# Kernel tuning notes

Hardware: AMD Instinct MI355X
Metric: run time of the kernel (lower is better)

Reference implementation:

```python
import jax, jax.numpy as jnp
import numpy as np

B, S, C, H, W = 4, 32, 128, 16, 32
HID = 128
DEPTH = 2


def conv2d_same(x, w, b):
    # x: [B,Cin,H,W], w: [Cout,Cin,3,3] -> [B,Cout,H,W]
    y = jax.lax.conv_general_dilated(x, w, window_strides=(1, 1), padding='SAME',
                                     dimension_numbers=('NCHW', 'OIHW', 'NCHW'))
    return y + b[None, :, None, None]


def setup_inputs() -> dict:
    key = jax.random.key(0)
    ks = jax.random.split(key, 12)
    sc = 0.02
    x = jax.random.normal(ks[0], (B, S, C, H, W), dtype=jnp.float32)
    # stacked ConvLSTM cell params; input to each cell is C==HID channels
    conv_w = sc * jax.random.normal(ks[1], (DEPTH, 4 * HID, C + HID, 3, 3), dtype=jnp.float32)
    conv_b = jnp.zeros((DEPTH, 4 * HID), dtype=jnp.float32)
    init_h = 0.01 * jax.random.normal(ks[2], (DEPTH, HID), dtype=jnp.float32)
    init_c = 0.01 * jax.random.normal(ks[3], (DEPTH, HID), dtype=jnp.float32)
    fc_w = sc * jax.random.normal(ks[4], (C, HID), dtype=jnp.float32)
    fc_b = jnp.zeros((C,), dtype=jnp.float32)
    fco_w = sc * jax.random.normal(ks[5], (1, C), dtype=jnp.float32)
    fco_b = jnp.zeros((1,), dtype=jnp.float32)
    fca_w = sc * jax.random.normal(ks[6], (1, C), dtype=jnp.float32)
    fca_b = jnp.zeros((1,), dtype=jnp.float32)
    return dict(x=x, conv_w=conv_w, conv_b=conv_b, init_h=init_h, init_c=init_c,
                fc_w=fc_w, fc_b=fc_b, fco_w=fco_w, fco_b=fco_b, fca_w=fca_w, fca_b=fca_b)


def _forward(x, conv_w, conv_b, init_h, init_c, fc_w, fc_b, fco_w, fco_b, fca_w, fca_b):
    b, s, c, h, w = x.shape
    hid = init_h.shape[1]
    xs = jnp.moveaxis(x, 1, 0)  # [S,B,C,H,W] time-major for scan
    for d in range(conv_w.shape[0]):  # fixed small depth loop
        wd, bd = conv_w[d], conv_b[d]
        h0 = jnp.broadcast_to(init_h[d][None, :, None, None], (b, hid, h, w))
        c0 = jnp.broadcast_to(init_c[d][None, :, None, None], (b, hid, h, w))

        def step(carry, x_t):
            hs, cs = carry
            z = conv2d_same(jnp.concatenate([x_t, hs], axis=1), wd, bd)
            zi, zf, zg, zo = jnp.split(z, 4, axis=1)  # gate order i,f,g,o
            cs = jax.nn.sigmoid(zf) * cs + jax.nn.sigmoid(zi) * jnp.tanh(zg)
            hs = jax.nn.sigmoid(zo) * jnp.tanh(cs)
            return (hs, cs), hs

        _, xs = jax.lax.scan(step, (h0, c0), xs)
    # global average pool over H,W then heads
    feat = jnp.moveaxis(xs.mean(axis=(3, 4)), 0, 1)  # [B,S,HID]
    feat = jax.nn.relu(feat @ fc_w.T + fc_b)
    offset = feat @ fco_w.T + fco_b  # [B,S,1]
    angle = feat @ fca_w.T + fca_b   # [B,S,1]
    return offset, angle


def reference(x, conv_w, conv_b, init_h, init_c, fc_w, fc_b, fco_w, fco_b, fca_w, fca_b):
    return _forward(x, conv_w, conv_b, init_h, init_c, fc_w, fc_b, fco_w, fco_b, fca_w, fca_b)
```

## Files before the change

kernel.cpp:

```cpp
#include <hip/hip_runtime.h>

#define BB 4
#define SS 32
#define CC 128
#define HH 16
#define WW 32
#define HID 128
#define DEPTH 2
#define CIN 256
#define COUT 512
#define K9 (CIN * 9)
#define KH 1152
#define KFULL (2 * KH)
#define HW (HH * WW)
#define MM (BB * HW)
#define ACT (BB * HW * 128)

typedef __attribute__((ext_vector_type(4))) float f32x4;
typedef __attribute__((ext_vector_type(8))) short bf16x8;

static __device__ __forceinline__ unsigned short f2bf(float f) {
    union { float f; unsigned u; } v; v.f = f;
    unsigned r = v.u + 0x7FFF + ((v.u >> 16) & 1);
    return (unsigned short)(r >> 16);
}
static __device__ __forceinline__ float bf2f(unsigned short h) {
    union { float f; unsigned u; } v; v.u = ((unsigned)h) << 16; return v.f;
}

__global__ void transpose_w_kernel(const float* __restrict__ w,
                                   unsigned short* __restrict__ wh) {
    int idx = blockIdx.x * 256 + threadIdx.x;
    if (idx >= DEPTH * K9 * COUT) return;
    int n = idx % COUT;
    int k = (idx / COUT) % K9;
    int d = idx / (COUT * K9);
    int cin = k / 9, tap = k % 9;
    float v = w[(((long)(d * COUT + n) * CIN + cin) * 9) + tap];
    int row = (cin < CC) ? (tap * CC + cin) : (KH + tap * HID + (cin - CC));
    int g = n >> 7, r = n & 127;
    int ng = (r >> 4) * 64 + g * 16 + (r & 15);
    wh[((long)d * COUT + ng) * KFULL + row] = f2bf(v);
}

__global__ void pack_x_kernel(const float* __restrict__ x,
                              unsigned* __restrict__ xh32) {
    __shared__ unsigned lh[128 * 33];
    const int tid = threadIdx.x;
    const int sb  = blockIdx.x;
    const int s   = sb >> 2;
    const int b   = sb & 3;
    const int hw0 = blockIdx.y * 64;
    const float* src = x + ((long)(b * SS + s) * CC) * HW;

    #pragma unroll
    for (int it = 0; it < 16; ++it) {
        int cc = it * 8 + (tid >> 5);
        int hw = (tid & 31) * 2;
        float2 v = *(const float2*)&src[cc * HW + hw0 + hw];
        unsigned short h0 = f2bf(v.x), h1 = f2bf(v.y);
        lh[cc * 33 + (hw >> 1)] = (unsigned)h0 | ((unsigned)h1 << 16);
    }
    __syncthreads();
    const unsigned short* lhs = (const unsigned short*)lh;
    #pragma unroll
    for (int it = 0; it < 16; ++it) {
        int hw = it * 4 + (tid >> 6);
        int c2 = tid & 63;
        unsigned short a0 = lhs[(2 * c2) * 66 + hw];
        unsigned short a1 = lhs[(2 * c2 + 1) * 66 + hw];
        long o = ((long)sb * HW + hw0 + hw) * 64 + c2;
        xh32[o] = (unsigned)a0 | ((unsigned)a1 << 16);
    }
}

__global__ void init_state_kernel(const float* __restrict__ ih, const float* __restrict__ ic,
                                  unsigned short* __restrict__ hh,
                                  float* __restrict__ c, int d) {
    int idx = blockIdx.x * 256 + threadIdx.x;
    int hid = idx & 127;
    hh[idx] = f2bf(ih[d * HID + hid]);
    c[idx] = ic[d * HID + hid];
}

__global__ void zero_kernel(unsigned* __restrict__ zp) { zp[threadIdx.x] = 0u; }

__launch_bounds__(256)
__global__ void step_dual(
    const unsigned short* __restrict__ x1h, const unsigned short* __restrict__ h1h,
    float* __restrict__ c1, unsigned short* __restrict__ o1h,
    const unsigned short* __restrict__ x2h, const unsigned short* __restrict__ h2h,
    float* __restrict__ c2, unsigned short* __restrict__ o2h,
    const unsigned short* __restrict__ wh,
    const float* __restrict__ bias, const unsigned short* __restrict__ zp,
    int do1, int do2)
{
    __shared__ __align__(16) unsigned short lds[2][16384];

    const int bid  = blockIdx.x;
    const int xcd  = bid & 7;
    const int q    = bid >> 3;
    const int mblk = q & 31;
    const int pp   = xcd + ((q >> 5) << 3);
    const int nblk = pp & 7;
    const int z    = pp >> 3;
    if (z == 0) { if (!do1) return; } else { if (!do2) return; }

    const unsigned short* axh = z ? x2h : x1h;
    const unsigned short* ahh = z ? h2h : h1h;
    const unsigned short* wph = wh + (long)z * COUT * KFULL;
    const float* bsel  = bias + z * COUT;
    float* csel        = z ? c2 : c1;
    unsigned short* ohh = z ? o2h : o1h;

    const int m0   = mblk * 64;
    const int n0g  = nblk * 64;
    const int hid0 = nblk * 16;
    const int tid  = threadIdx.x;
    const int lane = tid & 63;
    const int wv   = tid >> 6;
    const int wm   = (wv >> 1) * 32;
    const int wn   = (wv & 1) * 32;
    const int b    = m0 >> 9;
    const int hwl  = m0 & 511;
    const int y0   = hwl >> 5;
    const long bhw = (long)b * HW;

    int sy_[4], sx_[4], ax_[4];
    long bro_[4];
    #pragma unroll
    for (int s = 0; s < 4; ++s) {
        int row = wv * 16 + s * 4 + (lane >> 4);
        int jx  = (lane & 15) ^ (row & 7);
        sx_[s] = row & 31;
        sy_[s] = y0 + (row >> 5);
        ax_[s] = jx * 8;
        bro_[s] = (long)(n0g + row) * KFULL + jx * 8;
    }

#define ISSUE(tt, pb) do {                                                        \
        const int _tt = (tt);                                                     \
        const int _tap = (_tt < 9) ? _tt : _tt - 9;                               \
        const unsigned short* _sh = (_tt < 9) ? axh : ahh;                        \
        const int _ky = _tap / 3 - 1;                                             \
        const int _kx = _tap - (_tap / 3) * 3 - 1;                                \
        const long _bk = (long)_tt * 128;                                         \
        _Pragma("unroll")                                                         \
        for (int _s = 0; _s < 4; ++_s) {                                          \
            int _yy = sy_[_s] + _ky, _xq = sx_[_s] + _kx;                         \
            bool _ok = (unsigned)_yy < (unsigned)HH && (unsigned)_xq < (unsigned)WW;\
            long _a = ((bhw + _yy * WW + _xq) << 7) + ax_[_s];                    \
            __builtin_amdgcn_global_load_lds(                                     \
                (const unsigned int*)(_ok ? _sh + _a : zp),                       \
                (unsigned int*)&lds[pb][wv * 2048 + _s * 512], 16, 0, 0);         \
            __builtin_amdgcn_global_load_lds(                                     \
                (const unsigned int*)(wph + bro_[_s] + _bk),                      \
                (unsigned int*)&lds[pb][8192 + wv * 2048 + _s * 512], 16, 0, 0);  \
        }                                                                         \
    } while (0)

    f32x4 acc00 = (f32x4){0.f,0.f,0.f,0.f};
    f32x4 acc01 = (f32x4){0.f,0.f,0.f,0.f};
    f32x4 acc10 = (f32x4){0.f,0.f,0.f,0.f};
    f32x4 acc11 = (f32x4){0.f,0.f,0.f,0.f};

    const int fr  = lane & 15;
    const int kqi = lane >> 4;
    const int am0 = wm + fr;
    const int am1 = wm + 16 + fr;
    const int bn0 = wn + fr;
    const int bn1 = wn + 16 + fr;

#define COMPUTE(P) do {                                                                   \
        const unsigned short* L = &lds[P][0];                                             \
        __builtin_amdgcn_s_setprio(1);                                                    \
        _Pragma("unroll")                                                                 \
        for (int s2 = 0; s2 < 4; ++s2) {                                                  \
            const int ca = s2 * 4 + kqi;                                 \
            bf16x8 fa0 = *(const bf16x8*)&L[am0 * 128 + ((ca ^ (am0 & 7)) << 3)];         \
            bf16x8 fa1 = *(const bf16x8*)&L[am1 * 128 + ((ca ^ (am1 & 7)) << 3)];         \
            bf16x8 fb0 = *(const bf16x8*)&L[8192 + bn0 * 128 + ((ca ^ (bn0 & 7)) << 3)];  \
            bf16x8 fb1 = *(const bf16x8*)&L[8192 + bn1 * 128 + ((ca ^ (bn1 & 7)) << 3)];  \
            acc00 = __builtin_amdgcn_mfma_f32_16x16x32_bf16(fa0, fb0, acc00, 0, 0, 0);    \
            acc01 = __builtin_amdgcn_mfma_f32_16x16x32_bf16(fa0, fb1, acc01, 0, 0, 0);    \
            acc10 = __builtin_amdgcn_mfma_f32_16x16x32_bf16(fa1, fb0, acc10, 0, 0, 0);    \
            acc11 = __builtin_amdgcn_mfma_f32_16x16x32_bf16(fa1, fb1, acc11, 0, 0, 0);    \
        }                                                                                 \
        __builtin_amdgcn_s_setprio(0);                                                    \
    } while (0)

    ISSUE(0, 0);
    __syncthreads();

    int p = 0;
    for (int tt = 0; tt < 18; ++tt) {
        if (tt + 1 < 18) ISSUE(tt + 1, 1 - p);
        COMPUTE(p);
        __syncthreads();
        p ^= 1;
    }

#undef ISSUE
#undef COMPUTE

    float* zt = (float*)&lds[0][0];
    {
        const int rm = (lane >> 4) * 4;
        const int cn = lane & 15;
        *(float4*)&zt[(wn + cn) * 68 + wm + rm]           = *(float4*)&acc00;
        *(float4*)&zt[(wn + 16 + cn) * 68 + wm + rm]      = *(float4*)&acc01;
        *(float4*)&zt[(wn + cn) * 68 + wm + 16 + rm]      = *(float4*)&acc10;
        *(float4*)&zt[(wn + 16 + cn) * 68 + wm + 16 + rm] = *(float4*)&acc11;
    }
    __syncthreads();

    {
        const int m    = tid & 63;
        const int jset = tid >> 6;
        float g[4][4];
        #pragma unroll
        for (int ji = 0; ji < 4; ++ji) {
            int jh = jset * 4 + ji;
            #pragma unroll
            for (int gi = 0; gi < 4; ++gi)
                g[ji][gi] = zt[(gi * 16 + jh) * 68 + m] + bsel[gi * 128 + hid0 + jh];
        }
        long base = ((long)b * HW + hwl + m) * 128 + hid0 + jset * 4;
        f32x4 cv = *(const f32x4*)&csel[base];
        float hv[4];
        #pragma unroll
        for (int ji = 0; ji < 4; ++ji) {
            float si = 1.f / (1.f + expf(-g[ji][0]));
            float sf = 1.f / (1.f + expf(-g[ji][1]));
            float so = 1.f / (1.f + expf(-g[ji][3]));
            float cs = sf * cv[ji] + si * tanhf(g[ji][2]);
            cv[ji] = cs;
            hv[ji] = so * tanhf(cs);
        }
        *(f32x4*)&csel[base] = cv;
        uint2 hp;
        hp.x = (unsigned)f2bf(hv[0]) | ((unsigned)f2bf(hv[1]) << 16);
        hp.y = (unsigned)f2bf(hv[2]) | ((unsigned)f2bf(hv[3]) << 16);
        *(uint2*)&ohh[base] = hp;
    }
}

__global__ void pool_kernel(const unsigned short* __restrict__ s2h,
                            float* __restrict__ pooled) {
    int bs = blockIdx.x;
    int j  = threadIdx.x;
    const unsigned short* ph = s2h + (long)bs * HW * 128 + j;
    float sum = 0.f;
    #pragma unroll 8
    for (int hw = 0; hw < HW; ++hw)
        sum += bf2f(ph[hw * 128]);
    pooled[bs * HID + j] = sum * (1.f / HW);
}

__global__ void head_kernel(const float* __restrict__ pooled,
                            const float* __restrict__ fc_w, const float* __restrict__ fc_b,
                            const float* __restrict__ fco_w, const float* __restrict__ fco_b,
                            const float* __restrict__ fca_w, const float* __restrict__ fca_b,
                            float* __restrict__ out) {
    int bs = blockIdx.x;
    int b  = bs / SS;
    int s  = bs % SS;
    int j  = threadIdx.x;
    const float* prow = pooled + (long)(s * BB + b) * HID;
    float acc = fc_b[j];
    #pragma unroll 4
    for (int k = 0; k < HID; ++k) acc += fc_w[j * HID + k] * prow[k];
    float f = fmaxf(acc, 0.f);
    __shared__ float ro[128], ra[128];
    ro[j] = f * fco_w[j];
    ra[j] = f * fca_w[j];
    __syncthreads();
    for (int off = 64; off; off >>= 1) {
        if (j < off) { ro[j] += ro[j + off]; ra[j] += ra[j + off]; }
        __syncthreads();
    }
    if (j == 0) {
        out[bs]           = ro[0] + fco_b[0];
        out[BB * SS + bs] = ra[0] + fca_b[0];
    }
}

extern "C" void kernel_launch(void* const* d_in, const int* in_sizes, int n_in,
                              void* d_out, int out_size, void* d_ws, size_t ws_size,
                              hipStream_t stream) {
    const float* x      = (const float*)d_in[0];
    const float* conv_w = (const float*)d_in[1];
    const float* conv_b = (const float*)d_in[2];
    const float* init_h = (const float*)d_in[3];
    const float* init_c = (const float*)d_in[4];
    const float* fc_w   = (const float*)d_in[5];
    const float* fc_b   = (const float*)d_in[6];
    const float* fco_w  = (const float*)d_in[7];
    const float* fco_b  = (const float*)d_in[8];
    const float* fca_w  = (const float*)d_in[9];
    const float* fca_b  = (const float*)d_in[10];
    float* out = (float*)d_out;

    unsigned short* wh  = (unsigned short*)d_ws;
    unsigned short* xph = wh  + (long)DEPTH * COUT * KFULL;
    unsigned short* s1h = xph + (long)SS * ACT;
    unsigned short* s2h = s1h + (long)SS * ACT;
    unsigned short* h1h = s2h + (long)SS * ACT;
    unsigned short* h2h = h1h + ACT;
    float* c1     = (float*)(h2h + ACT);
    float* c2     = c1 + ACT;
    float* pooled = c2 + ACT;
    unsigned short* zp = (unsigned short*)(pooled + SS * BB * HID);

    transpose_w_kernel<<<(DEPTH * K9 * COUT + 255) / 256, 256, 0, stream>>>(conv_w, wh);
    pack_x_kernel<<<dim3(SS * BB, HW / 64), 256, 0, stream>>>(x, (unsigned*)xph);
    init_state_kernel<<<ACT / 256, 256, 0, stream>>>(init_h, init_c, h1h, c1, 0);
    init_state_kernel<<<ACT / 256, 256, 0, stream>>>(init_h, init_c, h2h, c2, 1);
    zero_kernel<<<1, 64, 0, stream>>>((unsigned*)zp);

    for (int t = 0; t <= SS; ++t) {
        int do1 = (t < SS) ? 1 : 0;
        int do2 = (t >= 1) ? 1 : 0;
        int t1 = (t < SS) ? t : SS - 1;
        int u2 = (t >= 1) ? t - 1 : 0;
        const unsigned short* ax1h = xph + (long)t1 * ACT;
        const unsigned short* ah1h = (t1 == 0) ? h1h : s1h + (long)(t1 - 1) * ACT;
        unsigned short* ao1h = s1h + (long)t1 * ACT;
        const unsigned short* ax2h = s1h + (long)u2 * ACT;
        const unsigned short* ah2h = (u2 == 0) ? h2h : s2h + (long)(u2 - 1) * ACT;
        unsigned short* ao2h = s2h + (long)u2 * ACT;
        step_dual<<<512, 256, 0, stream>>>(
            ax1h, ah1h, c1, ao1h,
            ax2h, ah2h, c2, ao2h,
            wh, conv_b, zp, do1, do2);
    }

    pool_kernel<<<SS * BB, 128, 0, stream>>>(s2h, pooled);
    head_kernel<<<BB * SS, 128, 0, stream>>>(pooled, fc_w, fc_b, fco_w, fco_b, fca_w, fca_b, out);
}
```

Baseline: 697.6 us.

## Double M tile to 128 rows per block and halve grid size

Each block now covers 128 output pixels instead of 64, and every wave computes a 64x32 sub-tile with 8 MFMA accumulators. Weight tiles loaded into LDS are reused across twice as many rows, and the grid shrinks from 512 to 256 blocks per timestep. The gate epilogue is restructured to process two passes over the larger tile. The cost is more LDS per block, more registers per wave, and fewer blocks to spread across the CUs.

```diff
diff --git a/kernel.cpp b/kernel.cpp
--- a/kernel.cpp
+++ b/kernel.cpp
@@ -95,13 +95,13 @@
     const float* __restrict__ bias, const unsigned short* __restrict__ zp,
     int do1, int do2)
 {
-    __shared__ __align__(16) unsigned short lds[2][16384];
+    __shared__ __align__(16) unsigned short lds[2][24576];
 
     const int bid  = blockIdx.x;
     const int xcd  = bid & 7;
     const int q    = bid >> 3;
-    const int mblk = q & 31;
-    const int pp   = xcd + ((q >> 5) << 3);
+    const int mblk = q & 15;
+    const int pp   = xcd + ((q >> 4) << 3);
     const int nblk = pp & 7;
     const int z    = pp >> 3;
     if (z == 0) { if (!do1) return; } else { if (!do2) return; }
@@ -113,28 +113,33 @@
     float* csel        = z ? c2 : c1;
     unsigned short* ohh = z ? o2h : o1h;
 
-    const int m0   = mblk * 64;
+    const int m0   = mblk * 128;
     const int n0g  = nblk * 64;
     const int hid0 = nblk * 16;
     const int tid  = threadIdx.x;
     const int lane = tid & 63;
     const int wv   = tid >> 6;
-    const int wm   = (wv >> 1) * 32;
+    const int wm   = (wv >> 1) * 64;
     const int wn   = (wv & 1) * 32;
     const int b    = m0 >> 9;
     const int hwl  = m0 & 511;
     const int y0   = hwl >> 5;
     const long bhw = (long)b * HW;
 
-    int sy_[4], sx_[4], ax_[4];
+    int asy_[8], asx_[8], aax_[8];
+    #pragma unroll
+    for (int s = 0; s < 8; ++s) {
+        int row = wv * 32 + s * 4 + (lane >> 4);
+        int jx  = (lane & 15) ^ (row & 7);
+        asx_[s] = row & 31;
+        asy_[s] = y0 + (row >> 5);
+        aax_[s] = jx * 8;
+    }
     long bro_[4];
     #pragma unroll
     for (int s = 0; s < 4; ++s) {
         int row = wv * 16 + s * 4 + (lane >> 4);
         int jx  = (lane & 15) ^ (row & 7);
-        sx_[s] = row & 31;
-        sy_[s] = y0 + (row >> 5);
-        ax_[s] = jx * 8;
         bro_[s] = (long)(n0g + row) * KFULL + jx * 8;
     }
 
@@ -146,47 +151,57 @@
         const int _kx = _tap - (_tap / 3) * 3 - 1;                                \
         const long _bk = (long)_tt * 128;                                         \
         _Pragma("unroll")                                                         \
-        for (int _s = 0; _s < 4; ++_s) {                                          \
-            int _yy = sy_[_s] + _ky, _xq = sx_[_s] + _kx;                         \
+        for (int _s = 0; _s < 8; ++_s) {                                          \
+            int _yy = asy_[_s] + _ky, _xq = asx_[_s] + _kx;                       \
             bool _ok = (unsigned)_yy < (unsigned)HH && (unsigned)_xq < (unsigned)WW;\
-            long _a = ((bhw + _yy * WW + _xq) << 7) + ax_[_s];                    \
+            long _a = ((bhw + _yy * WW + _xq) << 7) + aax_[_s];                   \
             __builtin_amdgcn_global_load_lds(                                     \
                 (const unsigned int*)(_ok ? _sh + _a : zp),                       \
-                (unsigned int*)&lds[pb][wv * 2048 + _s * 512], 16, 0, 0);         \
+                (unsigned int*)&lds[pb][wv * 4096 + _s * 512], 16, 0, 0);         \
+        }                                                                         \
+        _Pragma("unroll")                                                         \
+        for (int _s = 0; _s < 4; ++_s) {                                          \
             __builtin_amdgcn_global_load_lds(                                     \
                 (const unsigned int*)(wph + bro_[_s] + _bk),                      \
-                (unsigned int*)&lds[pb][8192 + wv * 2048 + _s * 512], 16, 0, 0);  \
+                (unsigned int*)&lds[pb][16384 + wv * 2048 + _s * 512], 16, 0, 0); \
         }                                                                         \
     } while (0)
 
-    f32x4 acc00 = (f32x4){0.f,0.f,0.f,0.f};
-    f32x4 acc01 = (f32x4){0.f,0.f,0.f,0.f};
-    f32x4 acc10 = (f32x4){0.f,0.f,0.f,0.f};
-    f32x4 acc11 = (f32x4){0.f,0.f,0.f,0.f};
+    f32x4 acc[4][2];
+    #pragma unroll
+    for (int i = 0; i < 4; ++i)
+        #pragma unroll
+        for (int j = 0; j < 2; ++j)
+            acc[i][j] = (f32x4){0.f,0.f,0.f,0.f};
 
     const int fr  = lane & 15;
     const int kqi = lane >> 4;
-    const int am0 = wm + fr;
-    const int am1 = wm + 16 + fr;
-    const int bn0 = wn + fr;
-    const int bn1 = wn + 16 + fr;
-
-#define COMPUTE(P) do {                                                                   \
-        const unsigned short* L = &lds[P][0];                                             \
-        __builtin_amdgcn_s_setprio(1);                                                    \
-        _Pragma("unroll")                                                                 \
-        for (int s2 = 0; s2 < 4; ++s2) {                                                  \
-            const int ca = s2 * 4 + kqi;                                 \
-            bf16x8 fa0 = *(const bf16x8*)&L[am0 * 128 + ((ca ^ (am0 & 7)) << 3)];         \
-            bf16x8 fa1 = *(const bf16x8*)&L[am1 * 128 + ((ca ^ (am1 & 7)) << 3)];         \
-            bf16x8 fb0 = *(const bf16x8*)&L[8192 + bn0 * 128 + ((ca ^ (bn0 & 7)) << 3)];  \
-            bf16x8 fb1 = *(const bf16x8*)&L[8192 + bn1 * 128 + ((ca ^ (bn1 & 7)) << 3)];  \
-            acc00 = __builtin_amdgcn_mfma_f32_16x16x32_bf16(fa0, fb0, acc00, 0, 0, 0);    \
-            acc01 = __builtin_amdgcn_mfma_f32_16x16x32_bf16(fa0, fb1, acc01, 0, 0, 0);    \
-            acc10 = __builtin_amdgcn_mfma_f32_16x16x32_bf16(fa1, fb0, acc10, 0, 0, 0);    \
-            acc11 = __builtin_amdgcn_mfma_f32_16x16x32_bf16(fa1, fb1, acc11, 0, 0, 0);    \
-        }                                                                                 \
-        __builtin_amdgcn_s_setprio(0);                                                    \
+    int amr[4], bnr[2];
+    #pragma unroll
+    for (int i = 0; i < 4; ++i) amr[i] = wm + i * 16 + fr;
+    #pragma unroll
+    for (int j = 0; j < 2; ++j) bnr[j] = wn + j * 16 + fr;
+
+#define COMPUTE(P) do {                                                                    \
+        const unsigned short* L = &lds[P][0];                                              \
+        __builtin_amdgcn_s_setprio(1);                                                     \
+        _Pragma("unroll")                                                                  \
+        for (int s2 = 0; s2 < 4; ++s2) {                                                   \
+            const int ca = s2 * 4 + kqi;                                  \
+            bf16x8 fa[4], fb[2];                                                           \
+            _Pragma("unroll")                                                              \
+            for (int i = 0; i < 4; ++i)                                                    \
+                fa[i] = *(const bf16x8*)&L[amr[i] * 128 + ((ca ^ (amr[i] & 7)) << 3)];     \
+            _Pragma("unroll")                                                              \
+            for (int j = 0; j < 2; ++j)                                                    \
+                fb[j] = *(const bf16x8*)&L[16384 + bnr[j] * 128 + ((ca ^ (bnr[j] & 7)) << 3)];\
+            _Pragma("unroll")                                                              \
+            for (int i = 0; i < 4; ++i)                                                    \
+                _Pragma("unroll")                                                          \
+                for (int j = 0; j < 2; ++j)                                                \
+                    acc[i][j] = __builtin_amdgcn_mfma_f32_16x16x32_bf16(fa[i], fb[j], acc[i][j], 0, 0, 0);\
+        }                                                                                  \
+        __builtin_amdgcn_s_setprio(0);                                                     \
     } while (0)
 
     ISSUE(0, 0);
@@ -207,25 +222,30 @@
     {
         const int rm = (lane >> 4) * 4;
         const int cn = lane & 15;
-        *(float4*)&zt[(wn + cn) * 68 + wm + rm]           = *(float4*)&acc00;
-        *(float4*)&zt[(wn + 16 + cn) * 68 + wm + rm]      = *(float4*)&acc01;
-        *(float4*)&zt[(wn + cn) * 68 + wm + 16 + rm]      = *(float4*)&acc10;
-        *(float4*)&zt[(wn + 16 + cn) * 68 + wm + 16 + rm] = *(float4*)&acc11;
+        #pragma unroll
+        for (int i = 0; i < 4; ++i)
+            #pragma unroll
+            for (int j = 0; j < 2; ++j)
+                *(float4*)&zt[(wn + j * 16 + cn) * 132 + wm + i * 16 + rm] = *(float4*)&acc[i][j];
     }
     __syncthreads();
 
-    {
-        const int m    = tid & 63;
-        const int jset = tid >> 6;
+    #pragma unroll
+    for (int i2 = 0; i2 < 2; ++i2) {
+        int e  = i2 * 256 + tid;
+        int m  = e & 127;
+        int jq = e >> 7;
+        jq = i2 * 2 + (e >> 8);
+        jq = e >> 7;
         float g[4][4];
         #pragma unroll
         for (int ji = 0; ji < 4; ++ji) {
-            int jh = jset * 4 + ji;
+            int jh = jq * 4 + ji;
             #pragma unroll
             for (int gi = 0; gi < 4; ++gi)
-                g[ji][gi] = zt[(gi * 16 + jh) * 68 + m] + bsel[gi * 128 + hid0 + jh];
+                g[ji][gi] = zt[(gi * 16 + jh) * 132 + m] + bsel[gi * 128 + hid0 + jh];
         }
-        long base = ((long)b * HW + hwl + m) * 128 + hid0 + jset * 4;
+        long base = ((long)b * HW + hwl + m) * 128 + hid0 + jq * 4;
         f32x4 cv = *(const f32x4*)&csel[base];
         float hv[4];
         #pragma unroll
@@ -329,7 +349,7 @@
         const unsigned short* ax2h = s1h + (long)u2 * ACT;
         const unsigned short* ah2h = (u2 == 0) ? h2h : s2h + (long)(u2 - 1) * ACT;
         unsigned short* ao2h = s2h + (long)u2 * ACT;
-        step_dual<<<512, 256, 0, stream>>>(
+        step_dual<<<256, 256, 0, stream>>>(
             ax1h, ah1h, c1, ao1h,
             ax2h, ah2h, c2, ao2h,
             wh, conv_b, zp, do1, do2);
```

New measurement: 886.8 us. +27.1%, slower.
